# Optimization experiments

Measured on AMD Instinct MI355X. Metric: run time of the kernel, lower is better.

The kernel has to match this reference:

```python
import jax, jax.numpy as jnp
import numpy as np

N_HEAD = 16
HEAD_DIM = 64
WINDOW = 256
ROPE_BASE = 10000.0


def _rope_cos_sin(seq_len, dtype):
    inv_freq = 1.0 / (ROPE_BASE ** (jnp.arange(0, HEAD_DIM, 2, dtype=jnp.float32) / HEAD_DIM))
    t = jnp.arange(seq_len, dtype=jnp.float32)
    freqs = jnp.outer(t, inv_freq)                      # [S, D/2]
    emb = jnp.concatenate([freqs, freqs], axis=-1)      # [S, D]
    return jnp.cos(emb).astype(dtype), jnp.sin(emb).astype(dtype)


def _rotate_half(x):
    x1, x2 = jnp.split(x, 2, axis=-1)
    return jnp.concatenate([-x2, x1], axis=-1)


def _apply_rope(x, cos, sin):
    # x: [B, H, S, D]; cos/sin: [S, D]
    return x * cos[None, None, :, :] + _rotate_half(x) * sin[None, None, :, :]


def setup_inputs() -> dict:
    key = jax.random.key(0)
    ks = jax.random.split(key, 5)
    B, S, E = 2, 2048, 1024
    scale = 1.0 / np.sqrt(E)
    return {
        "x": jax.random.normal(ks[0], (B, S, E), dtype=jnp.float32),
        "Wq": jax.random.normal(ks[1], (E, E), dtype=jnp.float32) * scale,
        "Wk": jax.random.normal(ks[2], (E, E), dtype=jnp.float32) * scale,
        "Wv": jax.random.normal(ks[3], (E, E), dtype=jnp.float32) * scale,
        "Wo": jax.random.normal(ks[4], (E, E), dtype=jnp.float32) * scale,
    }


def reference(x, Wq, Wk, Wv, Wo):
    B, S, E = x.shape
    # QKV projections (nn.Linear: x @ W.T), split heads -> [B, H, S, D]
    def proj(W):
        return (x @ W.T).reshape(B, S, N_HEAD, HEAD_DIM).transpose(0, 2, 1, 3)
    q, k, v = proj(Wq), proj(Wk), proj(Wv)

    cos, sin = _rope_cos_sin(S, x.dtype)
    q = _apply_rope(q, cos, sin)
    k = _apply_rope(k, cos, sin)

    # banded causal mask: attend iff 0 <= i - j < WINDOW
    pos = jnp.arange(S)
    rel = pos[:, None] - pos[None, :]
    allowed = (rel >= 0) & (rel < WINDOW)                # [S, S]

    scale = 1.0 / np.sqrt(HEAD_DIM)
    att = jnp.einsum("bhqd,bhkd->bhqk", q, k) * scale    # [B, H, S, S]
    att = jnp.where(allowed[None, None, :, :], att, -jnp.inf)
    att = jax.nn.softmax(att.astype(jnp.float32), axis=-1).astype(x.dtype)
    y = jnp.einsum("bhqk,bhkd->bhqd", att, v)
    y = y.transpose(0, 2, 1, 3).reshape(B, S, E)
    return y @ Wo.T
```

## Files before the change

kernel.cpp:

```cpp
#include <hip/hip_runtime.h>
#include <cstdint>
#include <cstddef>

#define AS1 __attribute__((address_space(1)))
#define AS3 __attribute__((address_space(3)))

typedef __attribute__((ext_vector_type(4))) float f32x4;
typedef __attribute__((ext_vector_type(8))) short bf16x8;
typedef unsigned short u16;
typedef unsigned int u32;

#define B_ 2
#define S_ 2048
#define E_ 1024
#define H_ 16
#define D_ 64
#define M_ 4096

__device__ __forceinline__ u16 f2bf(float f) {
  union { float f; u32 u; } v; v.f = f;
  u32 u = v.u;
  u32 r = (u + 0x7FFFu + ((u >> 16) & 1u)) >> 16;
  return (u16)r;
}
__device__ __forceinline__ float bf2f(u16 h) {
  union { u32 u; float f; } v; v.u = ((u32)h) << 16;
  return v.f;
}

__device__ __forceinline__ void gl2lds16(const void* g, void* l) {
  __builtin_amdgcn_global_load_lds((const AS1 void*)g, (AS3 void*)l, 16, 0, 0);
}

__global__ __launch_bounds__(256) void prep_kernel(
    const float* __restrict__ x, const float* __restrict__ wq,
    const float* __restrict__ wk, const float* __restrict__ wv,
    const float* __restrict__ wo,
    u16* __restrict__ xb, u16* __restrict__ wqkv, u16* __restrict__ wob,
    float* __restrict__ ctab, float* __restrict__ stab)
{
  int idx = blockIdx.x * 256 + threadIdx.x;
  const int NX4 = (M_ * E_) / 4;
  const int NW4 = (E_ * E_) / 4;
  const int CONV_TOTAL = NX4 + 4 * NW4;
  if (idx < CONV_TOTAL) {
    const float* src; u16* dst; int off;
    if (idx < NX4)                { src = x;  dst = xb;              off = idx; }
    else if (idx < NX4 + NW4)     { src = wq; dst = wqkv;            off = idx - NX4; }
    else if (idx < NX4 + 2 * NW4) { src = wk; dst = wqkv + E_ * E_;  off = idx - NX4 - NW4; }
    else if (idx < NX4 + 3 * NW4) { src = wv; dst = wqkv + 2 * E_ * E_; off = idx - NX4 - 2 * NW4; }
    else                          { src = wo; dst = wob;             off = idx - NX4 - 3 * NW4; }
    float4 v = reinterpret_cast<const float4*>(src)[off];
    ushort4 o;
    o.x = f2bf(v.x); o.y = f2bf(v.y); o.z = f2bf(v.z); o.w = f2bf(v.w);
    reinterpret_cast<ushort4*>(dst)[off] = o;
  } else if (idx < CONV_TOTAL + S_ * 32) {
    int e = idx - CONV_TOTAL;
    int s = e >> 5, i = e & 31;
    double invf = pow(10000.0, -(double)i / 32.0);
    double ang = (double)s * invf;
    ctab[e] = (float)cos(ang);
    stab[e] = (float)sin(ang);
  }
}

template <int MODE>
__global__ __launch_bounds__(256) void gemm_bt(
    const u16* __restrict__ A, const u16* __restrict__ Bm,
    u16* __restrict__ q_out, u16* __restrict__ k_out, u16* __restrict__ vt_out,
    float* __restrict__ f_out)
{
  __shared__ __align__(16) u16 lA[128 * 64];
  __shared__ __align__(16) u16 lB[128 * 64];
  const int tid = threadIdx.x;
  const int w = tid >> 6, l = tid & 63;
  const int lr = l & 15, lg = l >> 4;
  const int mt = blockIdx.y, nt = blockIdx.x;
  const int woffm = (w >> 1) * 64, woffn = (w & 1) * 64;

  const int srow = l >> 3;
  const int scol = ((l & 7) ^ srow) * 8;
  const u16* Abase = A + (size_t)(mt * 128) * 1024;
  const u16* Bbase = Bm + (size_t)(nt * 128) * 1024;

  f32x4 acc[4][4];
#pragma unroll
  for (int i = 0; i < 4; ++i)
#pragma unroll
    for (int j = 0; j < 4; ++j) acc[i][j] = (f32x4){0.f, 0.f, 0.f, 0.f};

  for (int kt = 0; kt < 1024; kt += 64) {
    __syncthreads();
#pragma unroll
    for (int i = 0; i < 4; ++i) {
      int ch = w * 4 + i;
      int row = ch * 8 + srow;
      gl2lds16(Abase + row * 1024 + kt + scol, &lA[ch * 512]);
      gl2lds16(Bbase + row * 1024 + kt + scol, &lB[ch * 512]);
    }
    __syncthreads();
#pragma unroll
    for (int kk = 0; kk < 2; ++kk) {
      bf16x8 av[4], bv[4];
#pragma unroll
      for (int mf = 0; mf < 4; ++mf) {
        int row = woffm + mf * 16 + lr;
        int byteoff = row * 128 + ((kk * 64 + lg * 16) ^ ((row & 7) << 4));
        av[mf] = *(const bf16x8*)((const char*)lA + byteoff);
      }
#pragma unroll
      for (int nf = 0; nf < 4; ++nf) {
        int row = woffn + nf * 16 + lr;
        int byteoff = row * 128 + ((kk * 64 + lg * 16) ^ ((row & 7) << 4));
        bv[nf] = *(const bf16x8*)((const char*)lB + byteoff);
      }
#pragma unroll
      for (int mf = 0; mf < 4; ++mf)
#pragma unroll
        for (int nf = 0; nf < 4; ++nf)
          acc[mf][nf] = __builtin_amdgcn_mfma_f32_16x16x32_bf16(
              av[mf], bv[nf], acc[mf][nf], 0, 0, 0);
    }
  }

  if (MODE == 0) {
#pragma unroll
    for (int mf = 0; mf < 4; ++mf) {
      int sbase = mt * 128 + woffm + mf * 16 + lg * 4;
      int b = sbase >> 11, s = sbase & 2047;
#pragma unroll
      for (int nf = 0; nf < 4; ++nf) {
        int n = nt * 128 + woffn + nf * 16 + lr;
        int wsel = n >> 10, r = n & 1023, hh = r >> 6, d = r & 63;
        if (wsel == 2) {
          ushort4 pk;
          pk.x = f2bf(acc[mf][nf][0]); pk.y = f2bf(acc[mf][nf][1]);
          pk.z = f2bf(acc[mf][nf][2]); pk.w = f2bf(acc[mf][nf][3]);
          *reinterpret_cast<ushort4*>(
              vt_out + ((size_t)(b * 16 + hh) * 64 + d) * 2048 + s) = pk;
        } else {
          u16* dst = (wsel == 0 ? q_out : k_out) +
                     ((size_t)(b * 16 + hh) * 2048) * 64 + d;
#pragma unroll
          for (int rr = 0; rr < 4; ++rr)
            dst[(size_t)(s + rr) * 64] = f2bf(acc[mf][nf][rr]);
        }
      }
    }
  } else {
#pragma unroll
    for (int mf = 0; mf < 4; ++mf) {
      int m = mt * 128 + woffm + mf * 16 + lg * 4;
#pragma unroll
      for (int nf = 0; nf < 4; ++nf) {
        int n = nt * 128 + woffn + nf * 16 + lr;
#pragma unroll
        for (int rr = 0; rr < 4; ++rr)
          f_out[(size_t)(m + rr) * 1024 + n] = acc[mf][nf][rr];
      }
    }
  }
}

__global__ __launch_bounds__(256) void rope_apply(
    u16* __restrict__ qb, u16* __restrict__ kb,
    const float* __restrict__ ctab, const float* __restrict__ stab)
{
  int tid = blockIdx.x * 256 + threadIdx.x;
  int d = tid & 31;
  int s = (tid >> 5) & 2047;
  int bh = tid >> 16;
  size_t base = ((size_t)bh * 2048 + s) * 64;
  float c = ctab[s * 32 + d], sn = stab[s * 32 + d];
  u16* qp = qb + base; u16* kp = kb + base;
  float q1 = bf2f(qp[d]), q2 = bf2f(qp[d + 32]);
  qp[d]      = f2bf(q1 * c - q2 * sn);
  qp[d + 32] = f2bf(q2 * c + q1 * sn);
  float k1 = bf2f(kp[d]), k2 = bf2f(kp[d + 32]);
  kp[d]      = f2bf(k1 * c - k2 * sn);
  kp[d + 32] = f2bf(k2 * c + k1 * sn);
}

__global__ __launch_bounds__(256) void attn_kernel(
    const u16* __restrict__ qb, const u16* __restrict__ kb,
    const u16* __restrict__ vt, u16* __restrict__ yb)
{
  int blk = blockIdx.x;
  int qt = blk & 31, h = (blk >> 5) & 15, b = blk >> 9;
  int w = threadIdx.x >> 6, l = threadIdx.x & 63;
  int lr = l & 15, lg = l >> 4;
  int qbase = qt * 64 + w * 16;

  const u16* Q  = qb + ((size_t)(b * 16 + h) * 2048) * 64;
  const u16* Kp = kb + ((size_t)(b * 16 + h) * 2048) * 64;
  const u16* Vp = vt + ((size_t)(b * 16 + h) * 64) * 2048;

  __shared__ __align__(16) u16 lds_p[4][16 * 40];
  u16* myp = &lds_p[w][0];

  bf16x8 aq0 = *(const bf16x8*)(Q + (size_t)(qbase + lr) * 64 + lg * 8);
  bf16x8 aq1 = *(const bf16x8*)(Q + (size_t)(qbase + lr) * 64 + 32 + lg * 8);

  f32x4 o[4];
#pragma unroll
  for (int i = 0; i < 4; ++i) o[i] = (f32x4){0.f, 0.f, 0.f, 0.f};
  float mrun[4], lrun[4];
#pragma unroll
  for (int r = 0; r < 4; ++r) { mrun[r] = -1e30f; lrun[r] = 0.f; }

  int kstart = qbase - 255; if (kstart < 0) kstart = 0;
  kstart &= ~31;
  int kend = qbase + 16;
  const float scale = 0.125f;

  for (int kt = kstart; kt < kend; kt += 32) {
    bf16x8 bk0a = *(const bf16x8*)(Kp + (size_t)(kt + lr) * 64 + lg * 8);
    bf16x8 bk0b = *(const bf16x8*)(Kp + (size_t)(kt + lr) * 64 + 32 + lg * 8);
    bf16x8 bk1a = *(const bf16x8*)(Kp + (size_t)(kt + 16 + lr) * 64 + lg * 8);
    bf16x8 bk1b = *(const bf16x8*)(Kp + (size_t)(kt + 16 + lr) * 64 + 32 + lg * 8);
    f32x4 s0 = (f32x4){0.f, 0.f, 0.f, 0.f};
    f32x4 s1 = (f32x4){0.f, 0.f, 0.f, 0.f};
    s0 = __builtin_amdgcn_mfma_f32_16x16x32_bf16(aq0, bk0a, s0, 0, 0, 0);
    s0 = __builtin_amdgcn_mfma_f32_16x16x32_bf16(aq1, bk0b, s0, 0, 0, 0);
    s1 = __builtin_amdgcn_mfma_f32_16x16x32_bf16(aq0, bk1a, s1, 0, 0, 0);
    s1 = __builtin_amdgcn_mfma_f32_16x16x32_bf16(aq1, bk1b, s1, 0, 0, 0);

    float p0[4], p1[4], sf[4];
#pragma unroll
    for (int r = 0; r < 4; ++r) {
      int q = qbase + lg * 4 + r;
      int k0 = kt + lr, k1 = k0 + 16;
      int r0 = q - k0, r1 = q - k1;
      float v0 = (r0 >= 0 && r0 < 256) ? s0[r] * scale : -1e30f;
      float v1 = (r1 >= 0 && r1 < 256) ? s1[r] * scale : -1e30f;
      float mx = fmaxf(v0, v1);
      mx = fmaxf(mx, __shfl_xor(mx, 1));
      mx = fmaxf(mx, __shfl_xor(mx, 2));
      mx = fmaxf(mx, __shfl_xor(mx, 4));
      mx = fmaxf(mx, __shfl_xor(mx, 8));
      float mnew = fmaxf(mrun[r], mx);
      float f = __expf(mrun[r] - mnew);
      mrun[r] = mnew;
      p0[r] = __expf(v0 - mnew);
      p1[r] = __expf(v1 - mnew);
      float sm = p0[r] + p1[r];
      sm += __shfl_xor(sm, 1);
      sm += __shfl_xor(sm, 2);
      sm += __shfl_xor(sm, 4);
      sm += __shfl_xor(sm, 8);
      lrun[r] = lrun[r] * f + sm;
      sf[r] = f;
    }
#pragma unroll
    for (int nf = 0; nf < 4; ++nf)
#pragma unroll
      for (int r = 0; r < 4; ++r) o[nf][r] *= sf[r];

#pragma unroll
    for (int r = 0; r < 4; ++r) {
      myp[(lg * 4 + r) * 40 + lr]      = f2bf(p0[r]);
      myp[(lg * 4 + r) * 40 + 16 + lr] = f2bf(p1[r]);
    }
    asm volatile("s_waitcnt lgkmcnt(0)" ::: "memory");
    bf16x8 pa = *(const bf16x8*)((const char*)myp + lr * 80 + lg * 16);
    asm volatile("s_waitcnt lgkmcnt(0)" ::: "memory");

#pragma unroll
    for (int df = 0; df < 4; ++df) {
      bf16x8 vv = *(const bf16x8*)(Vp + (size_t)(df * 16 + lr) * 2048 + kt + lg * 8);
      o[df] = __builtin_amdgcn_mfma_f32_16x16x32_bf16(pa, vv, o[df], 0, 0, 0);
    }
  }

#pragma unroll
  for (int r = 0; r < 4; ++r) lrun[r] = 1.f / lrun[r];
#pragma unroll
  for (int df = 0; df < 4; ++df)
#pragma unroll
    for (int r = 0; r < 4; ++r) {
      int s = qbase + lg * 4 + r;
      int d = df * 16 + lr;
      yb[((size_t)(b * 2048 + s)) * 1024 + h * 64 + d] = f2bf(o[df][r] * lrun[r]);
    }
}

extern "C" void kernel_launch(void* const* d_in, const int* in_sizes, int n_in,
                              void* d_out, int out_size, void* d_ws, size_t ws_size,
                              hipStream_t stream) {
  const float* x  = (const float*)d_in[0];
  const float* wq = (const float*)d_in[1];
  const float* wk = (const float*)d_in[2];
  const float* wv = (const float*)d_in[3];
  const float* wo = (const float*)d_in[4];

  char* ws = (char*)d_ws;
  const size_t MB = 1u << 20;
  if (ws_size < 49 * MB) return;
  u16*   xb   = (u16*)(ws);
  u16*   wqkv = (u16*)(ws + 8 * MB);
  u16*   wob  = (u16*)(ws + 14 * MB);
  u16*   qb   = (u16*)(ws + 16 * MB);
  u16*   kb   = (u16*)(ws + 24 * MB);
  u16*   vt   = (u16*)(ws + 32 * MB);
  u16*   yb   = (u16*)(ws + 40 * MB);
  float* ct   = (float*)(ws + 48 * MB);
  float* st   = (float*)(ws + 48 * MB + 256 * 1024);
  float* out  = (float*)d_out;

  prep_kernel<<<8448, 256, 0, stream>>>(x, wq, wk, wv, wo, xb, wqkv, wob, ct, st);
  gemm_bt<0><<<dim3(24, 32), 256, 0, stream>>>(xb, wqkv, qb, kb, vt, nullptr);
  rope_apply<<<8192, 256, 0, stream>>>(qb, kb, ct, st);
  attn_kernel<<<1024, 256, 0, stream>>>(qb, kb, vt, yb);
  gemm_bt<1><<<dim3(8, 32), 256, 0, stream>>>(yb, wob, nullptr, nullptr, nullptr, out);
}
```

Measured before the change: 186.9 us.

## Fuse RoPE into QKV GEMM epilogue and defer softmax rescaling in attention

Removes the separate rope_apply kernel by rotating Q/K in the QKV GEMM epilogue, reading interleaved cos/sin pairs. Rotated rows are staged through LDS so each row goes out as coalesced 16-byte stores instead of scattered 2-byte writes. In attention, the running-max rescale is skipped unless some score exceeds the current max by more than 8, and the row-sum shuffle reduction moves out of the loop to the end. This saves a kernel launch, a full Q/K read-modify-write pass and per-iteration shuffles, at the cost of a wave-uniform branch and slightly looser numerical bounds on exp.

```diff
diff --git a/kernel.cpp b/kernel.cpp
--- a/kernel.cpp
+++ b/kernel.cpp
@@ -6,6 +6,7 @@
 #define AS3 __attribute__((address_space(3)))
 
 typedef __attribute__((ext_vector_type(4))) float f32x4;
+typedef __attribute__((ext_vector_type(2))) float f32x2;
 typedef __attribute__((ext_vector_type(8))) short bf16x8;
 typedef unsigned short u16;
 typedef unsigned int u32;
@@ -37,7 +38,7 @@
     const float* __restrict__ wk, const float* __restrict__ wv,
     const float* __restrict__ wo,
     u16* __restrict__ xb, u16* __restrict__ wqkv, u16* __restrict__ wob,
-    float* __restrict__ ctab, float* __restrict__ stab)
+    float* __restrict__ cstab)
 {
   int idx = blockIdx.x * 256 + threadIdx.x;
   const int NX4 = (M_ * E_) / 4;
@@ -59,8 +60,8 @@
     int s = e >> 5, i = e & 31;
     double invf = pow(10000.0, -(double)i / 32.0);
     double ang = (double)s * invf;
-    ctab[e] = (float)cos(ang);
-    stab[e] = (float)sin(ang);
+    cstab[e * 2]     = (float)cos(ang);
+    cstab[e * 2 + 1] = (float)sin(ang);
   }
 }
 
@@ -68,10 +69,11 @@
 __global__ __launch_bounds__(256) void gemm_bt(
     const u16* __restrict__ A, const u16* __restrict__ Bm,
     u16* __restrict__ q_out, u16* __restrict__ k_out, u16* __restrict__ vt_out,
-    float* __restrict__ f_out)
+    float* __restrict__ f_out, const float* __restrict__ cstab)
 {
-  __shared__ __align__(16) u16 lA[128 * 64];
-  __shared__ __align__(16) u16 lB[128 * 64];
+  __shared__ __align__(16) u16 smem[17408];
+  u16* lA = smem;
+  u16* lB = smem + 8192;
   const int tid = threadIdx.x;
   const int w = tid >> 6, l = tid & 63;
   const int lr = l & 15, lg = l >> 4;
@@ -123,28 +125,57 @@
     }
   }
 
+  __syncthreads();
+
   if (MODE == 0) {
-#pragma unroll
-    for (int mf = 0; mf < 4; ++mf) {
-      int sbase = mt * 128 + woffm + mf * 16 + lg * 4;
-      int b = sbase >> 11, s = sbase & 2047;
-#pragma unroll
-      for (int nf = 0; nf < 4; ++nf) {
-        int n = nt * 128 + woffn + nf * 16 + lr;
-        int wsel = n >> 10, r = n & 1023, hh = r >> 6, d = r & 63;
-        if (wsel == 2) {
+    int n0 = nt * 128 + woffn;
+    int wsel = n0 >> 10;
+    int hh = (n0 >> 6) & 15;
+    int stile = mt * 128 + woffm;
+    int b = stile >> 11;
+    int s0 = stile & 2047;
+    if (wsel == 2) {
+#pragma unroll
+      for (int mf = 0; mf < 4; ++mf) {
+        int s = s0 + mf * 16 + lg * 4;
+#pragma unroll
+        for (int nf = 0; nf < 4; ++nf) {
+          int d = nf * 16 + lr;
           ushort4 pk;
           pk.x = f2bf(acc[mf][nf][0]); pk.y = f2bf(acc[mf][nf][1]);
           pk.z = f2bf(acc[mf][nf][2]); pk.w = f2bf(acc[mf][nf][3]);
           *reinterpret_cast<ushort4*>(
               vt_out + ((size_t)(b * 16 + hh) * 64 + d) * 2048 + s) = pk;
-        } else {
-          u16* dst = (wsel == 0 ? q_out : k_out) +
-                     ((size_t)(b * 16 + hh) * 2048) * 64 + d;
-#pragma unroll
-          for (int rr = 0; rr < 4; ++rr)
-            dst[(size_t)(s + rr) * 64] = f2bf(acc[mf][nf][rr]);
         }
+      }
+    } else {
+      u16* lt = smem + w * (64 * 68);
+      const f32x2* cst = (const f32x2*)cstab;
+#pragma unroll
+      for (int mf = 0; mf < 4; ++mf) {
+        int sl = mf * 16 + lg * 4;
+#pragma unroll
+        for (int rr = 0; rr < 4; ++rr) {
+          int s = s0 + sl + rr;
+#pragma unroll
+          for (int nf = 0; nf < 2; ++nf) {
+            int i = nf * 16 + lr;
+            f32x2 cs = cst[s * 32 + i];
+            float a = acc[mf][nf][rr], bb = acc[mf][nf + 2][rr];
+            lt[(sl + rr) * 68 + i]      = f2bf(a * cs.x - bb * cs.y);
+            lt[(sl + rr) * 68 + 32 + i] = f2bf(bb * cs.x + a * cs.y);
+          }
+        }
+      }
+      asm volatile("s_waitcnt lgkmcnt(0)" ::: "memory");
+      u16* gout = (wsel == 0 ? q_out : k_out) +
+                  ((size_t)(b * 16 + hh) * 2048 + s0) * 64;
+      int rl = l >> 3, cc = l & 7;
+#pragma unroll
+      for (int it = 0; it < 8; ++it) {
+        int row = it * 8 + rl;
+        bf16x8 v = *(const bf16x8*)(lt + row * 68 + cc * 8);
+        *(bf16x8*)(gout + (size_t)row * 64 + cc * 8) = v;
       }
     }
   } else {
@@ -160,25 +191,6 @@
       }
     }
   }
-}
-
-__global__ __launch_bounds__(256) void rope_apply(
-    u16* __restrict__ qb, u16* __restrict__ kb,
-    const float* __restrict__ ctab, const float* __restrict__ stab)
-{
-  int tid = blockIdx.x * 256 + threadIdx.x;
-  int d = tid & 31;
-  int s = (tid >> 5) & 2047;
-  int bh = tid >> 16;
-  size_t base = ((size_t)bh * 2048 + s) * 64;
-  float c = ctab[s * 32 + d], sn = stab[s * 32 + d];
-  u16* qp = qb + base; u16* kp = kb + base;
-  float q1 = bf2f(qp[d]), q2 = bf2f(qp[d + 32]);
-  qp[d]      = f2bf(q1 * c - q2 * sn);
-  qp[d + 32] = f2bf(q2 * c + q1 * sn);
-  float k1 = bf2f(kp[d]), k2 = bf2f(kp[d + 32]);
-  kp[d]      = f2bf(k1 * c - k2 * sn);
-  kp[d + 32] = f2bf(k2 * c + k1 * sn);
 }
 
 __global__ __launch_bounds__(256) void attn_kernel(
@@ -204,9 +216,9 @@
   f32x4 o[4];
 #pragma unroll
   for (int i = 0; i < 4; ++i) o[i] = (f32x4){0.f, 0.f, 0.f, 0.f};
-  float mrun[4], lrun[4];
-#pragma unroll
-  for (int r = 0; r < 4; ++r) { mrun[r] = -1e30f; lrun[r] = 0.f; }
+  float mrun[4], lsum[4];
+#pragma unroll
+  for (int r = 0; r < 4; ++r) { mrun[r] = -1e30f; lsum[r] = 0.f; }
 
   int kstart = qbase - 255; if (kstart < 0) kstart = 0;
   kstart &= ~31;
@@ -225,7 +237,7 @@
     s1 = __builtin_amdgcn_mfma_f32_16x16x32_bf16(aq0, bk1a, s1, 0, 0, 0);
     s1 = __builtin_amdgcn_mfma_f32_16x16x32_bf16(aq1, bk1b, s1, 0, 0, 0);
 
-    float p0[4], p1[4], sf[4];
+    float p0[4], p1[4];
 #pragma unroll
     for (int r = 0; r < 4; ++r) {
       int q = qbase + lg * 4 + r;
@@ -233,28 +245,24 @@
       int r0 = q - k0, r1 = q - k1;
       float v0 = (r0 >= 0 && r0 < 256) ? s0[r] * scale : -1e30f;
       float v1 = (r1 >= 0 && r1 < 256) ? s1[r] * scale : -1e30f;
-      float mx = fmaxf(v0, v1);
-      mx = fmaxf(mx, __shfl_xor(mx, 1));
-      mx = fmaxf(mx, __shfl_xor(mx, 2));
-      mx = fmaxf(mx, __shfl_xor(mx, 4));
-      mx = fmaxf(mx, __shfl_xor(mx, 8));
-      float mnew = fmaxf(mrun[r], mx);
-      float f = __expf(mrun[r] - mnew);
-      mrun[r] = mnew;
-      p0[r] = __expf(v0 - mnew);
-      p1[r] = __expf(v1 - mnew);
-      float sm = p0[r] + p1[r];
-      sm += __shfl_xor(sm, 1);
-      sm += __shfl_xor(sm, 2);
-      sm += __shfl_xor(sm, 4);
-      sm += __shfl_xor(sm, 8);
-      lrun[r] = lrun[r] * f + sm;
-      sf[r] = f;
-    }
-#pragma unroll
-    for (int nf = 0; nf < 4; ++nf)
-#pragma unroll
-      for (int r = 0; r < 4; ++r) o[nf][r] *= sf[r];
+      float pmax = fmaxf(v0, v1);
+      if (!__all(pmax <= mrun[r] + 8.0f)) {
+        float mx = pmax;
+        mx = fmaxf(mx, __shfl_xor(mx, 1));
+        mx = fmaxf(mx, __shfl_xor(mx, 2));
+        mx = fmaxf(mx, __shfl_xor(mx, 4));
+        mx = fmaxf(mx, __shfl_xor(mx, 8));
+        float mnew = fmaxf(mrun[r], mx);
+        float f = __expf(mrun[r] - mnew);
+        mrun[r] = mnew;
+        lsum[r] *= f;
+#pragma unroll
+        for (int nf = 0; nf < 4; ++nf) o[nf][r] *= f;
+      }
+      p0[r] = __expf(v0 - mrun[r]);
+      p1[r] = __expf(v1 - mrun[r]);
+      lsum[r] += p0[r] + p1[r];
+    }
 
 #pragma unroll
     for (int r = 0; r < 4; ++r) {
@@ -272,8 +280,16 @@
     }
   }
 
-#pragma unroll
-  for (int r = 0; r < 4; ++r) lrun[r] = 1.f / lrun[r];
+  float lrun[4];
+#pragma unroll
+  for (int r = 0; r < 4; ++r) {
+    float sm = lsum[r];
+    sm += __shfl_xor(sm, 1);
+    sm += __shfl_xor(sm, 2);
+    sm += __shfl_xor(sm, 4);
+    sm += __shfl_xor(sm, 8);
+    lrun[r] = 1.f / sm;
+  }
 #pragma unroll
   for (int df = 0; df < 4; ++df)
 #pragma unroll
@@ -303,13 +319,11 @@
   u16*   kb   = (u16*)(ws + 24 * MB);
   u16*   vt   = (u16*)(ws + 32 * MB);
   u16*   yb   = (u16*)(ws + 40 * MB);
-  float* ct   = (float*)(ws + 48 * MB);
-  float* st   = (float*)(ws + 48 * MB + 256 * 1024);
+  float* cst  = (float*)(ws + 48 * MB);
   float* out  = (float*)d_out;
 
-  prep_kernel<<<8448, 256, 0, stream>>>(x, wq, wk, wv, wo, xb, wqkv, wob, ct, st);
-  gemm_bt<0><<<dim3(24, 32), 256, 0, stream>>>(xb, wqkv, qb, kb, vt, nullptr);
-  rope_apply<<<8192, 256, 0, stream>>>(qb, kb, ct, st);
+  prep_kernel<<<8448, 256, 0, stream>>>(x, wq, wk, wv, wo, xb, wqkv, wob, cst);
+  gemm_bt<0><<<dim3(24, 32), 256, 0, stream>>>(xb, wqkv, qb, kb, vt, nullptr, cst);
   attn_kernel<<<1024, 256, 0, stream>>>(qb, kb, vt, yb);
-  gemm_bt<1><<<dim3(8, 32), 256, 0, stream>>>(yb, wob, nullptr, nullptr, nullptr, out);
-}
+  gemm_bt<1><<<dim3(8, 32), 256, 0, stream>>>(yb, wob, nullptr, nullptr, nullptr, out, nullptr);
+}
```

Measured after the change: 190.1 us. Within noise of the previous version (+1.7%).
